# Kernel tuning notes

Measured on AMD Instinct MI355X. Metric: run time of the kernel, lower is better.

The kernel has to match this reference:

```python
import jax, jax.numpy as jnp
import numpy as np

B, D, N, S = 4096, 768, 8192, 4  # batch, embedding_dim, len(y)==cat rows, source_size


def setup_inputs() -> dict:
    key = jax.random.key(0)
    k1, k2, k3, k4 = jax.random.split(key, 4)
    batch_x = jax.random.normal(k1, (B, D), dtype=jnp.float32)
    cat = jax.random.normal(k2, (N, D), dtype=jnp.float32)
    y = jax.random.randint(k3, (N,), 0, 2, dtype=jnp.int32)
    # phi_srcs: xavier-uniform-like scale for (D, 1) params, stacked as [S, D]
    phi = jax.random.normal(k4, (S, D), dtype=jnp.float32) * 0.05
    bias = jnp.zeros((1,), dtype=jnp.float32)
    return {"batch_x": batch_x, "cat": cat, "y": y, "phi": phi, "bias": bias}


def reference(batch_x, cat, y, phi, bias):
    # con[n, b] = cat[n] . batch_x[b]   -> [N, B]
    con = jnp.einsum('nd,bd->nb', cat, batch_x)
    # F.normalize(con, p=4, dim=0): divide each column by its 4-norm (eps=1e-12)
    norm4 = jnp.power(jnp.sum(jnp.abs(con) ** 4, axis=0), 0.25)
    con = con / jnp.maximum(norm4, 1e-12)
    # softmax over all N rows (dim=0), per batch column
    con = jax.nn.softmax(con, axis=0)
    # chunk into S sources along the N axis: psi [S, N/S, B]
    psi = con.reshape(S, N // S, B)
    yf = y.astype(jnp.float32).reshape(S, N // S)  # y chunks [S, N/S]
    # theta_s = exp(x @ phi_s): [S, B]  (unnormalized, as in the original output path)
    theta = jnp.exp(jnp.einsum('bd,sd->sb', batch_x, phi))
    # per-source: sum_n y[s,n] * psi[s,n,b], then scale by theta[s,b]; sum over sources
    sum_matrix = jnp.sum(jnp.einsum('sn,snb->sb', yf, psi) * theta, axis=0)  # [B]
    y_hat = jax.nn.sigmoid(sum_matrix + bias)  # bias [1] broadcasts -> [B]
    return y_hat
```

## Files before the change

### kernel.cpp

```cpp
#include <hip/hip_runtime.h>
#include <hip/hip_bf16.h>
#include <stdint.h>
#include <math.h>

#define Bdim 4096
#define Ddim 768
#define Ndim 8192
#define Sdim 4

typedef __attribute__((ext_vector_type(4))) float floatx4;
typedef __attribute__((ext_vector_type(8))) int int8v;
typedef __attribute__((ext_vector_type(4))) int int4v;

__device__ inline int pack_fp8x4(float4 v) {
  int r = __builtin_amdgcn_cvt_pk_fp8_f32(v.x, v.y, 0, 0);
  r = __builtin_amdgcn_cvt_pk_fp8_f32(v.z, v.w, r, 1);
  return r;
}

__device__ __forceinline__ void gl_lds16(const void* g, void* lds_base) {
  __builtin_amdgcn_global_load_lds(
      (const __attribute__((address_space(1))) unsigned int*)g,
      (__attribute__((address_space(3))) unsigned int*)lds_base, 16, 0, 0);
}

__global__ void convert_kernel(const float* __restrict__ x,
                               const float* __restrict__ cat,
                               const float* __restrict__ phi,
                               unsigned char* __restrict__ xq,
                               unsigned char* __restrict__ catq,
                               float* __restrict__ stats,
                               float* __restrict__ theta) {
  int gid = blockIdx.x * blockDim.x + threadIdx.x;
  int stride = gridDim.x * blockDim.x;
  const int nx4 = (Bdim * Ddim) / 4;
  const int nc4 = (Ndim * Ddim) / 4;
  for (int i = gid; i < nx4; i += stride)
    ((int*)xq)[i] = pack_fp8x4(((const float4*)x)[i]);
  for (int i = gid; i < nc4; i += stride)
    ((int*)catq)[i] = pack_fp8x4(((const float4*)cat)[i]);
  if (gid < 6 * Bdim) stats[gid] = 0.0f;

  int gw = gid >> 6;
  int lane = threadIdx.x & 63;
  if (gw < Bdim) {
    const float4* xr4 = (const float4*)(x + (size_t)gw * Ddim);
    const float4* ph4 = (const float4*)phi;
    const int D4 = Ddim / 4;
    float a0 = 0.f, a1 = 0.f, a2 = 0.f, a3 = 0.f;
#pragma unroll
    for (int d4 = lane; d4 < D4; d4 += 64) {
      float4 xv = xr4[d4];
      float4 p0 = ph4[d4];
      float4 p1 = ph4[D4 + d4];
      float4 p2 = ph4[2 * D4 + d4];
      float4 p3 = ph4[3 * D4 + d4];
      a0 = fmaf(xv.x, p0.x, fmaf(xv.y, p0.y, fmaf(xv.z, p0.z, fmaf(xv.w, p0.w, a0))));
      a1 = fmaf(xv.x, p1.x, fmaf(xv.y, p1.y, fmaf(xv.z, p1.z, fmaf(xv.w, p1.w, a1))));
      a2 = fmaf(xv.x, p2.x, fmaf(xv.y, p2.y, fmaf(xv.z, p2.z, fmaf(xv.w, p2.w, a2))));
      a3 = fmaf(xv.x, p3.x, fmaf(xv.y, p3.y, fmaf(xv.z, p3.z, fmaf(xv.w, p3.w, a3))));
    }
#pragma unroll
    for (int off = 32; off > 0; off >>= 1) {
      a0 += __shfl_down(a0, off);
      a1 += __shfl_down(a1, off);
      a2 += __shfl_down(a2, off);
      a3 += __shfl_down(a3, off);
    }
    if (lane == 0) {
      theta[gw] = __expf(a0);
      theta[Bdim + gw] = __expf(a1);
      theta[2 * Bdim + gw] = __expf(a2);
      theta[3 * Bdim + gw] = __expf(a3);
    }
  }
}

__global__ __launch_bounds__(256) void gemm_bt_kernel(
    const unsigned char* __restrict__ A,
    const unsigned char* __restrict__ Bm,
    unsigned int* __restrict__ Cw,
    float* __restrict__ s4) {
  __shared__ unsigned char As[128 * 128];
  __shared__ unsigned char Bs[128 * 128];

  const int tid = threadIdx.x;
  const int wave = tid >> 6;
  const int lane = tid & 63;
  const int quad = lane >> 4;
  const int l16 = lane & 15;
  const int wm = (wave & 1) * 64;
  const int wn = (wave >> 1) * 64;
  const int m0 = blockIdx.x * 128;
  const int n0 = blockIdx.y * 128;

  floatx4 acc[4][4];
#pragma unroll
  for (int i = 0; i < 4; ++i)
#pragma unroll
    for (int j = 0; j < 4; ++j) acc[i][j] = (floatx4){0.f, 0.f, 0.f, 0.f};

  const unsigned char* a_src[4];
  const unsigned char* b_src[4];
#pragma unroll
  for (int i = 0; i < 4; ++i) {
    int p = tid + 256 * i;
    int row = ((p >> 6) << 3) + (p & 7);
    int colb = ((p >> 3) & 7) * 16;
    a_src[i] = A + (size_t)(m0 + row) * Ddim + colb;
    b_src[i] = Bm + (size_t)(n0 + row) * Ddim + colb;
  }
  const int wbase = (wave * 64) * 16;

#pragma unroll
  for (int i = 0; i < 4; ++i) {
    gl_lds16(a_src[i], &As[wbase + i * 4096]);
    gl_lds16(b_src[i], &Bs[wbase + i * 4096]);
  }
  __syncthreads();

  for (int kk = 0; kk < 6; ++kk) {
    int8v af[4], bf[4];
#pragma unroll
    for (int mi = 0; mi < 4; ++mi) {
      int r = wm + mi * 16 + l16;
      int base = ((r >> 3) << 10) + quad * 256 + (r & 7) * 16;
      int4v lo = *(const int4v*)(&As[base]);
      int4v hi = *(const int4v*)(&As[base + 128]);
      af[mi] = __builtin_shufflevector(lo, hi, 0, 1, 2, 3, 4, 5, 6, 7);
    }
#pragma unroll
    for (int ni = 0; ni < 4; ++ni) {
      int r = wn + ni * 16 + l16;
      int base = ((r >> 3) << 10) + quad * 256 + (r & 7) * 16;
      int4v lo = *(const int4v*)(&Bs[base]);
      int4v hi = *(const int4v*)(&Bs[base + 128]);
      bf[ni] = __builtin_shufflevector(lo, hi, 0, 1, 2, 3, 4, 5, 6, 7);
    }
#pragma unroll
    for (int mi = 0; mi < 4; ++mi)
#pragma unroll
      for (int ni = 0; ni < 4; ++ni)
        acc[mi][ni] = __builtin_amdgcn_mfma_scale_f32_16x16x128_f8f6f4(
            af[mi], bf[ni], acc[mi][ni], 0, 0,
            0, 0x7f7f7f7f,
            0, 0x7f7f7f7f);

    __syncthreads();

    if (kk < 5) {
      const int k0 = (kk + 1) * 128;
#pragma unroll
      for (int i = 0; i < 4; ++i) {
        gl_lds16(a_src[i] + k0, &As[wbase + i * 4096]);
        gl_lds16(b_src[i] + k0, &Bs[wbase + i * 4096]);
      }
      __syncthreads();
    }
  }

  float cs4[4] = {0.f, 0.f, 0.f, 0.f};
#pragma unroll
  for (int mi = 0; mi < 4; ++mi)
#pragma unroll
    for (int ni = 0; ni < 4; ++ni) {
      int g = (m0 + wm + mi * 16) / 4 + quad;
      int col = n0 + wn + ni * 16 + l16;
      floatx4 a = acc[mi][ni];
      int w = __builtin_amdgcn_cvt_pk_fp8_f32(a[0], a[1], 0, 0);
      w = __builtin_amdgcn_cvt_pk_fp8_f32(a[2], a[3], w, 1);
      Cw[(size_t)g * Bdim + col] = (unsigned int)w;
#pragma unroll
      for (int rr = 0; rr < 4; ++rr) {
        float c2 = a[rr] * a[rr];
        cs4[ni] += c2 * c2;
      }
    }
#pragma unroll
  for (int ni = 0; ni < 4; ++ni) {
    float v = cs4[ni];
    v += __shfl_xor(v, 16);
    v += __shfl_xor(v, 32);
    if (quad == 0) atomicAdd(&s4[n0 + wn + ni * 16 + l16], v);
  }
}

__global__ void expsum_kernel(const unsigned int* __restrict__ conq,
                              const float* __restrict__ s4,
                              const int* __restrict__ y,
                              float* __restrict__ denom,
                              float* __restrict__ numer) {
  int b = blockIdx.x * 256 + threadIdx.x;
  int g0 = blockIdx.y * 16;
  int src = (g0 * 4) / (Ndim / Sdim);

  float inv = 1.0f / fmaxf(sqrtf(sqrtf(s4[b])), 1e-12f);
  float inv2 = inv * 1.4426950408889634f;
  const unsigned int* p = conq + (size_t)g0 * Bdim + b;
  float dsum = 0.f, nsum = 0.f;
#pragma unroll 4
  for (int i = 0; i < 16; ++i) {
    unsigned int w = p[(size_t)i * Bdim];
    int4 yv = *(const int4*)(y + 4 * (g0 + i));
    float e0 = exp2f(__builtin_amdgcn_cvt_f32_fp8(w, 0) * inv2);
    float e1 = exp2f(__builtin_amdgcn_cvt_f32_fp8(w, 1) * inv2);
    float e2 = exp2f(__builtin_amdgcn_cvt_f32_fp8(w, 2) * inv2);
    float e3 = exp2f(__builtin_amdgcn_cvt_f32_fp8(w, 3) * inv2);
    dsum += e0 + e1 + e2 + e3;
    nsum += e0 * (float)yv.x + e1 * (float)yv.y + e2 * (float)yv.z +
            e3 * (float)yv.w;
  }
  atomicAdd(&denom[b], dsum);
  atomicAdd(&numer[src * Bdim + b], nsum);
}

__global__ void finalize_kernel(const float* __restrict__ denom,
                                const float* __restrict__ numer,
                                const float* __restrict__ theta,
                                const float* __restrict__ bias,
                                float* __restrict__ out) {
  int b = blockIdx.x * 256 + threadIdx.x;
  float acc = 0.f;
#pragma unroll
  for (int si = 0; si < Sdim; ++si)
    acc += numer[si * Bdim + b] * theta[si * Bdim + b];
  float z = acc / denom[b] + bias[0];
  out[b] = 1.0f / (1.0f + __expf(-z));
}

extern "C" void kernel_launch(void* const* d_in, const int* in_sizes, int n_in,
                              void* d_out, int out_size, void* d_ws,
                              size_t ws_size, hipStream_t stream) {
  const float* batch_x = (const float*)d_in[0];
  const float* cat = (const float*)d_in[1];
  const int* y = (const int*)d_in[2];
  const float* phi = (const float*)d_in[3];
  const float* bias = (const float*)d_in[4];
  float* out = (float*)d_out;

  char* ws = (char*)d_ws;
  unsigned char* catq = (unsigned char*)ws;
  unsigned char* xq = catq + (size_t)Ndim * Ddim;
  unsigned int* conq = (unsigned int*)(xq + (size_t)Bdim * Ddim);
  float* stats = (float*)((unsigned char*)conq + (size_t)Ndim * Bdim);
  float* s4 = stats;
  float* denom = s4 + Bdim;
  float* numer = denom + Bdim;
  float* theta = stats + 6 * Bdim;

  convert_kernel<<<2048, 256, 0, stream>>>(batch_x, cat, phi, xq, catq, stats,
                                           theta);

  dim3 g2(Ndim / 128, Bdim / 128);
  gemm_bt_kernel<<<g2, 256, 0, stream>>>(catq, xq, conq, s4);

  dim3 g3(Bdim / 256, 128);
  expsum_kernel<<<g3, 256, 0, stream>>>(conq, s4, y, denom, numer);

  finalize_kernel<<<Bdim / 256, 256, 0, stream>>>(denom, numer, theta, bias,
                                                  out);
}
```

Measured before the change: 155.4 us.

## Double-buffer LDS tiles in FP8 GEMM to overlap global loads with MFMA

Splits the A and B shared-memory tiles into two buffers and prefetches the next K-tile one stage ahead, using explicit vmcnt waits and raw barriers in place of __syncthreads. The goal is to hide global-to-LDS load latency behind the MFMA work of the current tile. LDS use doubles to 64KB per block, which may reduce occupancy. The hand-counted vmcnt waits must match the number of outstanding loads for the result to stay correct.

```diff
diff --git a/kernel.cpp b/kernel.cpp
--- a/kernel.cpp
+++ b/kernel.cpp
@@ -81,8 +81,8 @@
     const unsigned char* __restrict__ Bm,
     unsigned int* __restrict__ Cw,
     float* __restrict__ s4) {
-  __shared__ unsigned char As[128 * 128];
-  __shared__ unsigned char Bs[128 * 128];
+  __shared__ unsigned char As[2][128 * 128];
+  __shared__ unsigned char Bs[2][128 * 128];
 
   const int tid = threadIdx.x;
   const int wave = tid >> 6;
@@ -114,27 +114,36 @@
 
 #pragma unroll
   for (int i = 0; i < 4; ++i) {
-    gl_lds16(a_src[i], &As[wbase + i * 4096]);
-    gl_lds16(b_src[i], &Bs[wbase + i * 4096]);
-  }
-  __syncthreads();
+    gl_lds16(a_src[i], &As[0][wbase + i * 4096]);
+    gl_lds16(b_src[i], &Bs[0][wbase + i * 4096]);
+  }
+#pragma unroll
+  for (int i = 0; i < 4; ++i) {
+    gl_lds16(a_src[i] + 128, &As[1][wbase + i * 4096]);
+    gl_lds16(b_src[i] + 128, &Bs[1][wbase + i * 4096]);
+  }
+  asm volatile("s_waitcnt vmcnt(8)" ::: "memory");
+  __builtin_amdgcn_sched_barrier(0);
+  __builtin_amdgcn_s_barrier();
+  __builtin_amdgcn_sched_barrier(0);
 
   for (int kk = 0; kk < 6; ++kk) {
+    const int cur = kk & 1;
     int8v af[4], bf[4];
 #pragma unroll
     for (int mi = 0; mi < 4; ++mi) {
       int r = wm + mi * 16 + l16;
       int base = ((r >> 3) << 10) + quad * 256 + (r & 7) * 16;
-      int4v lo = *(const int4v*)(&As[base]);
-      int4v hi = *(const int4v*)(&As[base + 128]);
+      int4v lo = *(const int4v*)(&As[cur][base]);
+      int4v hi = *(const int4v*)(&As[cur][base + 128]);
       af[mi] = __builtin_shufflevector(lo, hi, 0, 1, 2, 3, 4, 5, 6, 7);
     }
 #pragma unroll
     for (int ni = 0; ni < 4; ++ni) {
       int r = wn + ni * 16 + l16;
       int base = ((r >> 3) << 10) + quad * 256 + (r & 7) * 16;
-      int4v lo = *(const int4v*)(&Bs[base]);
-      int4v hi = *(const int4v*)(&Bs[base + 128]);
+      int4v lo = *(const int4v*)(&Bs[cur][base]);
+      int4v hi = *(const int4v*)(&Bs[cur][base + 128]);
       bf[ni] = __builtin_shufflevector(lo, hi, 0, 1, 2, 3, 4, 5, 6, 7);
     }
 #pragma unroll
@@ -146,16 +155,24 @@
             0, 0x7f7f7f7f,
             0, 0x7f7f7f7f);
 
-    __syncthreads();
-
     if (kk < 5) {
-      const int k0 = (kk + 1) * 128;
-#pragma unroll
-      for (int i = 0; i < 4; ++i) {
-        gl_lds16(a_src[i] + k0, &As[wbase + i * 4096]);
-        gl_lds16(b_src[i] + k0, &Bs[wbase + i * 4096]);
+      __builtin_amdgcn_sched_barrier(0);
+      __builtin_amdgcn_s_barrier();
+      __builtin_amdgcn_sched_barrier(0);
+      if (kk < 4) {
+        const int k0 = (kk + 2) * 128;
+#pragma unroll
+        for (int i = 0; i < 4; ++i) {
+          gl_lds16(a_src[i] + k0, &As[cur][wbase + i * 4096]);
+          gl_lds16(b_src[i] + k0, &Bs[cur][wbase + i * 4096]);
+        }
+        asm volatile("s_waitcnt vmcnt(8)" ::: "memory");
+      } else {
+        asm volatile("s_waitcnt vmcnt(0)" ::: "memory");
       }
-      __syncthreads();
+      __builtin_amdgcn_sched_barrier(0);
+      __builtin_amdgcn_s_barrier();
+      __builtin_amdgcn_sched_barrier(0);
     }
   }
 
```

New measurement: 160.6 us. +3.3%, slower.
